# Performance work log

Hardware: AMD Instinct MI355X
Metric: run time of the kernel (lower is better)

## Reference

```python
import jax, jax.numpy as jnp
import numpy as np
from jax import lax

T, H = 4096, 2048          # tokens, hidden_size
E, K = 64, 8               # n_routed_experts, top_k
I = 512                    # moe_intermediate_size
IS = 512                   # shared intermediate = moe_intermediate_size * n_shared_experts
ROUTED_SCALING = 2.5


def setup_inputs() -> dict:
    key = jax.random.key(0)
    ks = jax.random.split(key, 6)
    return {
        "hidden_states": jax.random.normal(ks[0], (T, H), jnp.float32),
        "gate_w": jax.random.normal(ks[1], (H, E), jnp.float32) * 0.05,
        "w13": jax.random.normal(ks[2], (E, H, 2 * I), jnp.float32) * 0.02,
        "w2": jax.random.normal(ks[3], (E, I, H), jnp.float32) * 0.02,
        "shared_w13": jax.random.normal(ks[4], (H, 2 * IS), jnp.float32) * 0.02,
        "shared_w2": jax.random.normal(ks[5], (IS, H), jnp.float32) * 0.02,
    }


def reference(hidden_states, gate_w, w13, w2, shared_w13, shared_w2):
    # --- router: sigmoid scoring, grouped top-k with 1 group == plain top-k ---
    logits = hidden_states @ gate_w                        # [T, E]
    scores = jax.nn.sigmoid(logits.astype(jnp.float32))
    topk_w, topk_ids = lax.top_k(scores, K)                # [T, K]
    topk_w = topk_w / jnp.sum(topk_w, axis=-1, keepdims=True)  # renormalize

    # --- dispatch: sort token-expert pairs by expert id, grouped GEMM ---
    flat_ids = topk_ids.reshape(-1)                        # [T*K]
    order = jnp.argsort(flat_ids)                          # pairs grouped by expert
    token_idx = order // K                                 # source token of each sorted pair
    x_sorted = hidden_states[token_idx]                    # [T*K, H]
    group_sizes = jnp.bincount(flat_ids, length=E).astype(jnp.int32)

    gu = lax.ragged_dot(x_sorted, w13, group_sizes)        # [T*K, 2I]
    h = jax.nn.silu(gu[:, :I]) * gu[:, I:]                 # SiluAndMul
    out_sorted = lax.ragged_dot(h, w2, group_sizes)        # [T*K, H]

    # --- combine: unsort, weight, sum over top-k ---
    inv = jnp.argsort(order)
    out_pairs = out_sorted[inv].reshape(T, K, H)
    routed = jnp.sum(out_pairs * topk_w[..., None].astype(out_pairs.dtype), axis=1)

    # --- shared expert MLP ---
    sg = hidden_states @ shared_w13                        # [T, 2*IS]
    shared = (jax.nn.silu(sg[:, :IS]) * sg[:, IS:]) @ shared_w2

    return routed * ROUTED_SCALING + shared
```

## Files before the change

### kernel.cpp

```cpp
#include <hip/hip_runtime.h>
#include <hip/hip_bf16.h>

#define T_TOK 4096
#define HD    2048
#define NE    64
#define TOPK  8
#define IMID  512
#define N13   1024
#define NPAIR (T_TOK*TOPK)
#define NROWS (NPAIR + T_TOK)
#define MAXT2 208
#define RSCALE 2.5f

typedef __attribute__((ext_vector_type(8))) __bf16 bf16x8;
typedef __attribute__((ext_vector_type(4))) __bf16 bf16x4;
typedef __attribute__((ext_vector_type(4))) float  f32x4;

__global__ __launch_bounds__(256) void init_kernel(float4* __restrict__ out4,
                                                   int* __restrict__ counts,
                                                   int* __restrict__ curs) {
  int gid = blockIdx.x * 256 + threadIdx.x;
  float4 z; z.x = z.y = z.z = z.w = 0.f;
  out4[gid] = z;
  if (gid < NE + 1) { counts[gid] = 0; curs[gid] = 0; }
}

__global__ __launch_bounds__(256) void cvt_kernel(const float4* __restrict__ hs4,
                                                  bf16x8* __restrict__ hb8) {
  int gid = blockIdx.x * 256 + threadIdx.x;
  float4 a = hs4[2 * gid], b = hs4[2 * gid + 1];
  bf16x8 v = { (__bf16)a.x, (__bf16)a.y, (__bf16)a.z, (__bf16)a.w,
               (__bf16)b.x, (__bf16)b.y, (__bf16)b.z, (__bf16)b.w };
  hb8[gid] = v;
}

__global__ __launch_bounds__(256) void logits_kernel(const float* __restrict__ hs,
                                                     const float* __restrict__ gw,
                                                     float* __restrict__ logits) {
  __shared__ float hsm[64][64];
  __shared__ float gwm[64][64];
  int tid = threadIdx.x;
  int tb = blockIdx.x * 64;
  int tok = tid & 63, kq = tid >> 6;
  int tq = (tid & 15) * 4, eq = (tid >> 4) * 4;
  float acc[4][4] = {};
  for (int c = 0; c < 32; ++c) {
    int kb = c * 64;
#pragma unroll
    for (int it = 0; it < 4; ++it) {
      int k4 = kq * 16 + it * 4;
      float4 f = *(const float4*)&hs[(size_t)(tb + tok) * HD + kb + k4];
      hsm[k4 + 0][tok] = f.x; hsm[k4 + 1][tok] = f.y;
      hsm[k4 + 2][tok] = f.z; hsm[k4 + 3][tok] = f.w;
      int q = tid + it * 256;
      int grow = q >> 4, gc = (q & 15) * 4;
      *(float4*)&gwm[grow][gc] = *(const float4*)&gw[(size_t)(kb + grow) * NE + gc];
    }
    __syncthreads();
#pragma unroll 8
    for (int k = 0; k < 64; ++k) {
      float4 g = *(const float4*)&gwm[k][eq];
      float h0 = hsm[k][tq + 0], h1 = hsm[k][tq + 1];
      float h2 = hsm[k][tq + 2], h3 = hsm[k][tq + 3];
      acc[0][0] += h0 * g.x; acc[0][1] += h0 * g.y; acc[0][2] += h0 * g.z; acc[0][3] += h0 * g.w;
      acc[1][0] += h1 * g.x; acc[1][1] += h1 * g.y; acc[1][2] += h1 * g.z; acc[1][3] += h1 * g.w;
      acc[2][0] += h2 * g.x; acc[2][1] += h2 * g.y; acc[2][2] += h2 * g.z; acc[2][3] += h2 * g.w;
      acc[3][0] += h3 * g.x; acc[3][1] += h3 * g.y; acc[3][2] += h3 * g.z; acc[3][3] += h3 * g.w;
    }
    __syncthreads();
  }
#pragma unroll
  for (int i = 0; i < 4; ++i)
#pragma unroll
    for (int j = 0; j < 4; ++j)
      logits[(size_t)(tb + tq + i) * NE + eq + j] = acc[i][j];
}

__global__ __launch_bounds__(256) void top8_kernel(const float* __restrict__ logits,
                                                   int* __restrict__ topk_id,
                                                   float* __restrict__ pair_w,
                                                   int* __restrict__ counts) {
  int lane = threadIdx.x & 63;
  int t = blockIdx.x * 4 + (threadIdx.x >> 6);
  float v = logits[(size_t)t * NE + lane];
  float s = 1.f / (1.f + __expf(-v));
  float cur = s, ssum = 0.f;
  int myid = 0; float myw = 0.f;
  for (int k = 0; k < TOPK; ++k) {
    float bv = cur; int bi = lane;
#pragma unroll
    for (int off = 32; off >= 1; off >>= 1) {
      float ov = __shfl_xor(bv, off);
      int   oi = __shfl_xor(bi, off);
      if (ov > bv || (ov == bv && oi < bi)) { bv = ov; bi = oi; }
    }
    ssum += bv;
    if (lane == k) { myid = bi; myw = bv; }
    if (lane == bi) cur = -1.f;
  }
  if (lane < TOPK) {
    topk_id[(size_t)t * TOPK + lane] = myid;
    pair_w[(size_t)t * TOPK + lane] = myw / ssum * RSCALE;
    atomicAdd(&counts[myid], 1);
  }
}

__global__ void scan_kernel(int* __restrict__ counts, int* __restrict__ offs,
                            int2* __restrict__ tiles) {
  if (threadIdx.x != 0) return;
  counts[NE] = T_TOK;
  int off = 0, tix = 0;
  for (int e = 0; e <= NE; ++e) {
    offs[e] = off;
    int c = counts[e];
    int nt = (c + 255) >> 8;
    for (int i = 0; i < nt; ++i) {
      int rr = c - i * 256; if (rr > 256) rr = 256;
      tiles[tix++] = make_int2(off + i * 256, (e << 16) | rr);
    }
    off += c;
  }
  for (; tix < MAXT2; ++tix) tiles[tix] = make_int2(0, 0);
}

__global__ __launch_bounds__(256) void scatter_kernel(const int* __restrict__ topk_id,
                                                      const float* __restrict__ pair_w,
                                                      const int* __restrict__ offs,
                                                      int* __restrict__ curs,
                                                      int* __restrict__ row_token,
                                                      float* __restrict__ row_w) {
  int p = blockIdx.x * 256 + threadIdx.x;
  int dst, t; float w;
  if (p < NPAIR) {
    t = p >> 3; int e = topk_id[p]; w = pair_w[p];
    dst = offs[e] + atomicAdd(&curs[e], 1);
  } else {
    t = p - NPAIR; w = 1.0f;
    dst = offs[NE] + t;
  }
  row_token[dst] = t;
  row_w[dst] = w;
}

__device__ __forceinline__ int swz(int row, int kbyte) {
  return row * 128 + (kbyte ^ ((row & 7) << 4));
}
__device__ __forceinline__ void barrier_lgkm() {
  asm volatile("s_waitcnt lgkmcnt(0)" ::: "memory");
  __builtin_amdgcn_s_barrier();
  __builtin_amdgcn_sched_barrier(0);
}
__device__ __forceinline__ void barrier_plain() {
  __builtin_amdgcn_sched_barrier(0);
  __builtin_amdgcn_s_barrier();
  __builtin_amdgcn_sched_barrier(0);
}
__device__ __forceinline__ void wait_vm0() {
  asm volatile("s_waitcnt vmcnt(0)" ::: "memory");
}
__device__ __forceinline__ void glds16(const void* g, void* l) {
  __builtin_amdgcn_global_load_lds((const __attribute__((address_space(1))) void*)g,
                                   (__attribute__((address_space(3))) void*)l, 16, 0, 0);
}
__device__ __forceinline__ void store_b4(__bf16* Bs, int c2, int kbyte, const float2* p) {
  bf16x4 c0 = { (__bf16)p[0].x, (__bf16)p[1].x, (__bf16)p[2].x, (__bf16)p[3].x };
  bf16x4 c1 = { (__bf16)p[0].y, (__bf16)p[1].y, (__bf16)p[2].y, (__bf16)p[3].y };
  *(bf16x4*)&Bs[swz(c2,     kbyte) >> 1] = c0;
  *(bf16x4*)&Bs[swz(c2 + 1, kbyte) >> 1] = c1;
}
__device__ __forceinline__ void store_b8(__bf16* Bs, int c2, int kbyte, const float2* p) {
  bf16x8 c0 = { (__bf16)p[0].x, (__bf16)p[1].x, (__bf16)p[2].x, (__bf16)p[3].x,
                (__bf16)p[4].x, (__bf16)p[5].x, (__bf16)p[6].x, (__bf16)p[7].x };
  bf16x8 c1 = { (__bf16)p[0].y, (__bf16)p[1].y, (__bf16)p[2].y, (__bf16)p[3].y,
                (__bf16)p[4].y, (__bf16)p[5].y, (__bf16)p[6].y, (__bf16)p[7].y };
  *(bf16x8*)&Bs[swz(c2,     kbyte) >> 1] = c0;
  *(bf16x8*)&Bs[swz(c2 + 1, kbyte) >> 1] = c1;
}

__global__ __launch_bounds__(512, 4) void gemm1_kernel(const __bf16* __restrict__ hidden_bf,
                                                       const float* __restrict__ w13,
                                                       const float* __restrict__ sw13,
                                                       const int* __restrict__ row_token,
                                                       const int2* __restrict__ tiles,
                                                       __bf16* __restrict__ hbuf) {
  int2 td = tiles[blockIdx.y];
  int rows = td.y & 0xFFFF;
  if (rows == 0) return;
  int e = td.y >> 16, row0 = td.x;
  const float* W = (e < NE) ? (w13 + (size_t)e * (HD * N13)) : sw13;
  int n0 = blockIdx.x * 64;

  __shared__ __bf16 As[256 * 64];
  __shared__ __bf16 Bgs[2][64 * 64];
  __shared__ __bf16 Bus[2][64 * 64];

  int tid = threadIdx.x;
  int lane = tid & 63, wv = tid >> 6;
  int l15 = lane & 15, lq = lane >> 4;

  int kswz = (((lane & 7) ^ (lane >> 3)) << 3);
  const __bf16* Abase[4];
#pragma unroll
  for (int i = 0; i < 4; ++i) {
    int grow = row0 + wv * 32 + i * 8 + (lane >> 3);
    if (grow >= NROWS) grow = NROWS - 1;
    Abase[i] = hidden_bf + (size_t)row_token[grow] * HD + kswz;
  }
  int c2 = (tid & 31) * 2, kq = tid >> 5;
  const float* Bg0 = W + (size_t)(kq * 4) * N13 + n0 + c2;
  const float* Bu0 = Bg0 + 512;

  float2 pg[4], pu[4];
#pragma unroll
  for (int r = 0; r < 4; ++r) {
    pg[r] = *(const float2*)(Bg0 + (size_t)r * N13);
    pu[r] = *(const float2*)(Bu0 + (size_t)r * N13);
  }
#pragma unroll
  for (int i = 0; i < 4; ++i)
    glds16(Abase[i], &As[wv * 2048 + i * 512]);
  store_b4(Bgs[0], c2, kq * 8, pg);
  store_b4(Bus[0], c2, kq * 8, pu);
  wait_vm0();
  barrier_lgkm();

  f32x4 accg[2][4], accu[2][4];
#pragma unroll
  for (int i = 0; i < 2; ++i)
#pragma unroll
    for (int j = 0; j < 4; ++j) { accg[i][j] = (f32x4)(0.f); accu[i][j] = (f32x4)(0.f); }

  for (int s = 0; s < 32; ++s) {
    int cur = s & 1;
    if (s + 1 < 32) {
      const float* Bg2 = Bg0 + (size_t)(s + 1) * 64 * N13;
      const float* Bu2 = Bu0 + (size_t)(s + 1) * 64 * N13;
#pragma unroll
      for (int r = 0; r < 4; ++r) {
        pg[r] = *(const float2*)(Bg2 + (size_t)r * N13);
        pu[r] = *(const float2*)(Bu2 + (size_t)r * N13);
      }
    }
#pragma unroll
    for (int kk = 0; kk < 2; ++kk) {
      int koff = kk * 64 + lq * 16;
      bf16x8 a0 = *(const bf16x8*)&As[swz(wv * 32 + l15,      koff) >> 1];
      bf16x8 a1 = *(const bf16x8*)&As[swz(wv * 32 + 16 + l15, koff) >> 1];
      {
        bf16x8 b[4];
#pragma unroll
        for (int j = 0; j < 4; ++j) b[j] = *(const bf16x8*)&Bgs[cur][swz(j * 16 + l15, koff) >> 1];
#pragma unroll
        for (int j = 0; j < 4; ++j) {
          accg[0][j] = __builtin_amdgcn_mfma_f32_16x16x32_bf16(a0, b[j], accg[0][j], 0, 0, 0);
          accg[1][j] = __builtin_amdgcn_mfma_f32_16x16x32_bf16(a1, b[j], accg[1][j], 0, 0, 0);
        }
      }
      {
        bf16x8 b[4];
#pragma unroll
        for (int j = 0; j < 4; ++j) b[j] = *(const bf16x8*)&Bus[cur][swz(j * 16 + l15, koff) >> 1];
#pragma unroll
        for (int j = 0; j < 4; ++j) {
          accu[0][j] = __builtin_amdgcn_mfma_f32_16x16x32_bf16(a0, b[j], accu[0][j], 0, 0, 0);
          accu[1][j] = __builtin_amdgcn_mfma_f32_16x16x32_bf16(a1, b[j], accu[1][j], 0, 0, 0);
        }
      }
    }
    barrier_plain();
    if (s + 1 < 32) {
#pragma unroll
      for (int i = 0; i < 4; ++i)
        glds16(Abase[i] + (s + 1) * 64, &As[wv * 2048 + i * 512]);
      store_b4(Bgs[cur ^ 1], c2, kq * 8, pg);
      store_b4(Bus[cur ^ 1], c2, kq * 8, pu);
      wait_vm0();
    }
    barrier_lgkm();
  }
#pragma unroll
  for (int mi = 0; mi < 2; ++mi) {
#pragma unroll
    for (int r = 0; r < 4; ++r) {
      int rl = wv * 32 + mi * 16 + lq * 4 + r;
      if (rl < rows) {
        size_t hrow = (size_t)(row0 + rl) * IMID;
#pragma unroll
        for (int j = 0; j < 4; ++j) {
          float g = accg[mi][j][r], u = accu[mi][j][r];
          float hv = g * u / (1.f + __expf(-g));
          hbuf[hrow + n0 + j * 16 + l15] = (__bf16)hv;
        }
      }
    }
  }
}

__global__ __launch_bounds__(512, 4) void gemm2_kernel(const __bf16* __restrict__ hbuf,
                                                       const float* __restrict__ w2,
                                                       const float* __restrict__ sw2,
                                                       const int* __restrict__ row_token,
                                                       const float* __restrict__ row_w,
                                                       const int2* __restrict__ tiles,
                                                       float* __restrict__ out) {
  int2 td = tiles[blockIdx.y];
  int rows = td.y & 0xFFFF;
  if (rows == 0) return;
  int e = td.y >> 16, row0 = td.x;
  const float* W = (e < NE) ? (w2 + (size_t)e * (IMID * HD)) : sw2;
  int n0 = blockIdx.x * 128;

  __shared__ __bf16 As[256 * 64];
  __shared__ __bf16 Bs[2][128 * 64];

  int tid = threadIdx.x;
  int lane = tid & 63, wv = tid >> 6, wr = wv >> 1, wc = wv & 1;
  int l15 = lane & 15, lq = lane >> 4;

  int kswz = (((lane & 7) ^ (lane >> 3)) << 3);
  const __bf16* Abase[4];
#pragma unroll
  for (int i = 0; i < 4; ++i) {
    int grow = row0 + wv * 32 + i * 8 + (lane >> 3);
    if (grow >= NROWS) grow = NROWS - 1;
    Abase[i] = hbuf + (size_t)grow * IMID + kswz;
  }

  int c2 = (tid & 63) * 2, kq = tid >> 6;
  const float* Bp0 = W + (size_t)(kq * 8) * HD + n0 + c2;

  float2 pb[8];
#pragma unroll
  for (int r = 0; r < 8; ++r) pb[r] = *(const float2*)(Bp0 + (size_t)r * HD);
#pragma unroll
  for (int i = 0; i < 4; ++i)
    glds16(Abase[i], &As[wv * 2048 + i * 512]);
  store_b8(Bs[0], c2, kq * 16, pb);
  wait_vm0();
  barrier_lgkm();

  f32x4 acc[4][4];
#pragma unroll
  for (int i = 0; i < 4; ++i)
#pragma unroll
    for (int j = 0; j < 4; ++j) acc[i][j] = (f32x4)(0.f);

  for (int s = 0; s < 8; ++s) {
    int cur = s & 1;
    if (s + 1 < 8) {
      const float* Bp2 = Bp0 + (size_t)(s + 1) * 64 * HD;
#pragma unroll
      for (int r = 0; r < 8; ++r) pb[r] = *(const float2*)(Bp2 + (size_t)r * HD);
    }
#pragma unroll
    for (int kk = 0; kk < 2; ++kk) {
      int koff = kk * 64 + lq * 16;
      bf16x8 a[4];
#pragma unroll
      for (int i = 0; i < 4; ++i)
        a[i] = *(const bf16x8*)&As[swz(wr * 64 + i * 16 + l15, koff) >> 1];
#pragma unroll
      for (int j = 0; j < 4; ++j) {
        bf16x8 b = *(const bf16x8*)&Bs[cur][swz(wc * 64 + j * 16 + l15, koff) >> 1];
#pragma unroll
        for (int i = 0; i < 4; ++i)
          acc[i][j] = __builtin_amdgcn_mfma_f32_16x16x32_bf16(a[i], b, acc[i][j], 0, 0, 0);
      }
    }
    barrier_plain();
    if (s + 1 < 8) {
#pragma unroll
      for (int i = 0; i < 4; ++i)
        glds16(Abase[i] + (s + 1) * 64, &As[wv * 2048 + i * 512]);
      store_b8(Bs[cur ^ 1], c2, kq * 16, pb);
      wait_vm0();
    }
    barrier_lgkm();
  }
#pragma unroll
  for (int i = 0; i < 4; ++i) {
#pragma unroll
    for (int r = 0; r < 4; ++r) {
      int rl = wr * 64 + i * 16 + lq * 4 + r;
      if (rl < rows) {
        int gr = row0 + rl;
        int tok = row_token[gr];
        float wgt = row_w[gr];
        float* orow = out + (size_t)tok * HD + n0 + wc * 64;
#pragma unroll
        for (int j = 0; j < 4; ++j)
          atomicAdd(&orow[j * 16 + l15], acc[i][j][r] * wgt);
      }
    }
  }
}

extern "C" void kernel_launch(void* const* d_in, const int* in_sizes, int n_in,
                              void* d_out, int out_size, void* d_ws, size_t ws_size,
                              hipStream_t stream) {
  const float* hidden = (const float*)d_in[0];
  const float* gate_w = (const float*)d_in[1];
  const float* w13    = (const float*)d_in[2];
  const float* w2     = (const float*)d_in[3];
  const float* sw13   = (const float*)d_in[4];
  const float* sw2    = (const float*)d_in[5];
  float* out = (float*)d_out;

  char* ws = (char*)d_ws;
  size_t off = 0;
  __bf16* hbuf      = (__bf16*)(ws + off); off += (size_t)NROWS * IMID * 2;
  __bf16* hidden_bf = (__bf16*)(ws + off); off += (size_t)T_TOK * HD * 2;
  float* logits  = (float*)(ws + off);  off += (size_t)T_TOK * NE * 4;
  int*   topk_id = (int*)(ws + off);    off += (size_t)NPAIR * 4;
  float* pair_w  = (float*)(ws + off);  off += (size_t)NPAIR * 4;
  int*   row_tok = (int*)(ws + off);    off += (size_t)NROWS * 4;
  float* row_w   = (float*)(ws + off);  off += (size_t)NROWS * 4;
  int*   counts  = (int*)(ws + off);    off += 512;
  int*   curs    = (int*)(ws + off);    off += 512;
  int*   offs    = (int*)(ws + off);    off += 512;
  int2*  tiles   = (int2*)(ws + off);   off += MAXT2 * 8;

  init_kernel<<<T_TOK * HD / 4 / 256, 256, 0, stream>>>((float4*)out, counts, curs);
  cvt_kernel<<<T_TOK * HD / 8 / 256, 256, 0, stream>>>((const float4*)hidden, (bf16x8*)hidden_bf);
  logits_kernel<<<T_TOK / 64, 256, 0, stream>>>(hidden, gate_w, logits);
  top8_kernel<<<T_TOK / 4, 256, 0, stream>>>(logits, topk_id, pair_w, counts);
  scan_kernel<<<1, 64, 0, stream>>>(counts, offs, tiles);
  scatter_kernel<<<NROWS / 256, 256, 0, stream>>>(topk_id, pair_w, offs, curs, row_tok, row_w);
  gemm1_kernel<<<dim3(8, MAXT2), 512, 0, stream>>>(hidden_bf, w13, sw13, row_tok, tiles, hbuf);
  gemm2_kernel<<<dim3(16, MAXT2), 512, 0, stream>>>(hbuf, w2, sw2, row_tok, row_w, tiles, out);
}
```

Measured before the change: 829.0 us.

## Triple-buffer A tiles, single barrier per k-step, retile gemm1 warps

```diff
diff --git a/kernel.cpp b/kernel.cpp
--- a/kernel.cpp
+++ b/kernel.cpp
@@ -145,19 +145,6 @@
 __device__ __forceinline__ int swz(int row, int kbyte) {
   return row * 128 + (kbyte ^ ((row & 7) << 4));
 }
-__device__ __forceinline__ void barrier_lgkm() {
-  asm volatile("s_waitcnt lgkmcnt(0)" ::: "memory");
-  __builtin_amdgcn_s_barrier();
-  __builtin_amdgcn_sched_barrier(0);
-}
-__device__ __forceinline__ void barrier_plain() {
-  __builtin_amdgcn_sched_barrier(0);
-  __builtin_amdgcn_s_barrier();
-  __builtin_amdgcn_sched_barrier(0);
-}
-__device__ __forceinline__ void wait_vm0() {
-  asm volatile("s_waitcnt vmcnt(0)" ::: "memory");
-}
 __device__ __forceinline__ void glds16(const void* g, void* l) {
   __builtin_amdgcn_global_load_lds((const __attribute__((address_space(1))) void*)g,
                                    (__attribute__((address_space(3))) void*)l, 16, 0, 0);
@@ -177,7 +164,7 @@
   *(bf16x8*)&Bs[swz(c2 + 1, kbyte) >> 1] = c1;
 }
 
-__global__ __launch_bounds__(512, 4) void gemm1_kernel(const __bf16* __restrict__ hidden_bf,
+__global__ __launch_bounds__(512, 2) void gemm1_kernel(const __bf16* __restrict__ hidden_bf,
                                                        const float* __restrict__ w13,
                                                        const float* __restrict__ sw13,
                                                        const int* __restrict__ row_token,
@@ -190,12 +177,13 @@
   const float* W = (e < NE) ? (w13 + (size_t)e * (HD * N13)) : sw13;
   int n0 = blockIdx.x * 64;
 
-  __shared__ __bf16 As[256 * 64];
+  __shared__ __bf16 As[3][256 * 64];
   __shared__ __bf16 Bgs[2][64 * 64];
   __shared__ __bf16 Bus[2][64 * 64];
 
   int tid = threadIdx.x;
   int lane = tid & 63, wv = tid >> 6;
+  int wrow = wv >> 1, wc = wv & 1;
   int l15 = lane & 15, lq = lane >> 4;
 
   int kswz = (((lane & 7) ^ (lane >> 3)) << 3);
@@ -216,22 +204,24 @@
     pg[r] = *(const float2*)(Bg0 + (size_t)r * N13);
     pu[r] = *(const float2*)(Bu0 + (size_t)r * N13);
   }
-#pragma unroll
-  for (int i = 0; i < 4; ++i)
-    glds16(Abase[i], &As[wv * 2048 + i * 512]);
   store_b4(Bgs[0], c2, kq * 8, pg);
   store_b4(Bus[0], c2, kq * 8, pu);
-  wait_vm0();
-  barrier_lgkm();
-
-  f32x4 accg[2][4], accu[2][4];
-#pragma unroll
-  for (int i = 0; i < 2; ++i)
-#pragma unroll
-    for (int j = 0; j < 4; ++j) { accg[i][j] = (f32x4)(0.f); accu[i][j] = (f32x4)(0.f); }
+#pragma unroll
+  for (int i = 0; i < 4; ++i) glds16(Abase[i],      &As[0][wv * 2048 + i * 512]);
+#pragma unroll
+  for (int i = 0; i < 4; ++i) glds16(Abase[i] + 64, &As[1][wv * 2048 + i * 512]);
+  asm volatile("s_waitcnt vmcnt(0) lgkmcnt(0)" ::: "memory");
+  __builtin_amdgcn_s_barrier();
+  __builtin_amdgcn_sched_barrier(0);
+
+  f32x4 accg[4][2], accu[4][2];
+#pragma unroll
+  for (int i = 0; i < 4; ++i)
+#pragma unroll
+    for (int j = 0; j < 2; ++j) { accg[i][j] = (f32x4)(0.f); accu[i][j] = (f32x4)(0.f); }
 
   for (int s = 0; s < 32; ++s) {
-    int cur = s & 1;
+    int cur = s % 3, nb = s & 1;
     if (s + 1 < 32) {
       const float* Bg2 = Bg0 + (size_t)(s + 1) * 64 * N13;
       const float* Bu2 = Bu0 + (size_t)(s + 1) * 64 * N13;
@@ -241,62 +231,63 @@
         pu[r] = *(const float2*)(Bu2 + (size_t)r * N13);
       }
     }
+    if (s + 2 < 32) {
+      int nxt3 = (s + 2) % 3;
+#pragma unroll
+      for (int i = 0; i < 4; ++i)
+        glds16(Abase[i] + (s + 2) * 64, &As[nxt3][wv * 2048 + i * 512]);
+    }
+    __builtin_amdgcn_sched_barrier(0);
 #pragma unroll
     for (int kk = 0; kk < 2; ++kk) {
       int koff = kk * 64 + lq * 16;
-      bf16x8 a0 = *(const bf16x8*)&As[swz(wv * 32 + l15,      koff) >> 1];
-      bf16x8 a1 = *(const bf16x8*)&As[swz(wv * 32 + 16 + l15, koff) >> 1];
-      {
-        bf16x8 b[4];
-#pragma unroll
-        for (int j = 0; j < 4; ++j) b[j] = *(const bf16x8*)&Bgs[cur][swz(j * 16 + l15, koff) >> 1];
-#pragma unroll
-        for (int j = 0; j < 4; ++j) {
-          accg[0][j] = __builtin_amdgcn_mfma_f32_16x16x32_bf16(a0, b[j], accg[0][j], 0, 0, 0);
-          accg[1][j] = __builtin_amdgcn_mfma_f32_16x16x32_bf16(a1, b[j], accg[1][j], 0, 0, 0);
+      bf16x8 a[4], bg[2], bu[2];
+#pragma unroll
+      for (int i = 0; i < 4; ++i)
+        a[i] = *(const bf16x8*)&As[cur][swz(wrow * 64 + i * 16 + l15, koff) >> 1];
+#pragma unroll
+      for (int j = 0; j < 2; ++j) {
+        bg[j] = *(const bf16x8*)&Bgs[nb][swz(wc * 32 + j * 16 + l15, koff) >> 1];
+        bu[j] = *(const bf16x8*)&Bus[nb][swz(wc * 32 + j * 16 + l15, koff) >> 1];
+      }
+#pragma unroll
+      for (int i = 0; i < 4; ++i)
+#pragma unroll
+        for (int j = 0; j < 2; ++j) {
+          accg[i][j] = __builtin_amdgcn_mfma_f32_16x16x32_bf16(a[i], bg[j], accg[i][j], 0, 0, 0);
+          accu[i][j] = __builtin_amdgcn_mfma_f32_16x16x32_bf16(a[i], bu[j], accu[i][j], 0, 0, 0);
+        }
+    }
+    if (s + 1 < 32) {
+      store_b4(Bgs[nb ^ 1], c2, kq * 8, pg);
+      store_b4(Bus[nb ^ 1], c2, kq * 8, pu);
+    }
+    if (s + 2 < 32)
+      asm volatile("s_waitcnt vmcnt(4) lgkmcnt(0)" ::: "memory");
+    else
+      asm volatile("s_waitcnt vmcnt(0) lgkmcnt(0)" ::: "memory");
+    __builtin_amdgcn_s_barrier();
+    __builtin_amdgcn_sched_barrier(0);
+  }
+#pragma unroll
+  for (int mi = 0; mi < 4; ++mi) {
+#pragma unroll
+    for (int r = 0; r < 4; ++r) {
+      int rl = wrow * 64 + mi * 16 + lq * 4 + r;
+      if (rl < rows) {
+        size_t hrow = (size_t)(row0 + rl) * IMID;
+#pragma unroll
+        for (int j = 0; j < 2; ++j) {
+          float g = accg[mi][j][r], u = accu[mi][j][r];
+          float hv = g * u / (1.f + __expf(-g));
+          hbuf[hrow + n0 + wc * 32 + j * 16 + l15] = (__bf16)hv;
         }
       }
-      {
-        bf16x8 b[4];
-#pragma unroll
-        for (int j = 0; j < 4; ++j) b[j] = *(const bf16x8*)&Bus[cur][swz(j * 16 + l15, koff) >> 1];
-#pragma unroll
-        for (int j = 0; j < 4; ++j) {
-          accu[0][j] = __builtin_amdgcn_mfma_f32_16x16x32_bf16(a0, b[j], accu[0][j], 0, 0, 0);
-          accu[1][j] = __builtin_amdgcn_mfma_f32_16x16x32_bf16(a1, b[j], accu[1][j], 0, 0, 0);
-        }
-      }
-    }
-    barrier_plain();
-    if (s + 1 < 32) {
-#pragma unroll
-      for (int i = 0; i < 4; ++i)
-        glds16(Abase[i] + (s + 1) * 64, &As[wv * 2048 + i * 512]);
-      store_b4(Bgs[cur ^ 1], c2, kq * 8, pg);
-      store_b4(Bus[cur ^ 1], c2, kq * 8, pu);
-      wait_vm0();
-    }
-    barrier_lgkm();
-  }
-#pragma unroll
-  for (int mi = 0; mi < 2; ++mi) {
-#pragma unroll
-    for (int r = 0; r < 4; ++r) {
-      int rl = wv * 32 + mi * 16 + lq * 4 + r;
-      if (rl < rows) {
-        size_t hrow = (size_t)(row0 + rl) * IMID;
-#pragma unroll
-        for (int j = 0; j < 4; ++j) {
-          float g = accg[mi][j][r], u = accu[mi][j][r];
-          float hv = g * u / (1.f + __expf(-g));
-          hbuf[hrow + n0 + j * 16 + l15] = (__bf16)hv;
-        }
-      }
-    }
-  }
-}
-
-__global__ __launch_bounds__(512, 4) void gemm2_kernel(const __bf16* __restrict__ hbuf,
+    }
+  }
+}
+
+__global__ __launch_bounds__(512, 2) void gemm2_kernel(const __bf16* __restrict__ hbuf,
                                                        const float* __restrict__ w2,
                                                        const float* __restrict__ sw2,
                                                        const int* __restrict__ row_token,
@@ -310,7 +301,7 @@
   const float* W = (e < NE) ? (w2 + (size_t)e * (IMID * HD)) : sw2;
   int n0 = blockIdx.x * 128;
 
-  __shared__ __bf16 As[256 * 64];
+  __shared__ __bf16 As[3][256 * 64];
   __shared__ __bf16 Bs[2][128 * 64];
 
   int tid = threadIdx.x;
@@ -332,50 +323,57 @@
   float2 pb[8];
 #pragma unroll
   for (int r = 0; r < 8; ++r) pb[r] = *(const float2*)(Bp0 + (size_t)r * HD);
+  store_b8(Bs[0], c2, kq * 16, pb);
+#pragma unroll
+  for (int i = 0; i < 4; ++i) glds16(Abase[i],      &As[0][wv * 2048 + i * 512]);
+#pragma unroll
+  for (int i = 0; i < 4; ++i) glds16(Abase[i] + 64, &As[1][wv * 2048 + i * 512]);
+  asm volatile("s_waitcnt vmcnt(0) lgkmcnt(0)" ::: "memory");
+  __builtin_amdgcn_s_barrier();
+  __builtin_amdgcn_sched_barrier(0);
+
+  f32x4 acc[4][4];
 #pragma unroll
   for (int i = 0; i < 4; ++i)
-    glds16(Abase[i], &As[wv * 2048 + i * 512]);
-  store_b8(Bs[0], c2, kq * 16, pb);
-  wait_vm0();
-  barrier_lgkm();
-
-  f32x4 acc[4][4];
-#pragma unroll
-  for (int i = 0; i < 4; ++i)
 #pragma unroll
     for (int j = 0; j < 4; ++j) acc[i][j] = (f32x4)(0.f);
 
   for (int s = 0; s < 8; ++s) {
-    int cur = s & 1;
+    int cur = s % 3, nb = s & 1;
     if (s + 1 < 8) {
       const float* Bp2 = Bp0 + (size_t)(s + 1) * 64 * HD;
 #pragma unroll
       for (int r = 0; r < 8; ++r) pb[r] = *(const float2*)(Bp2 + (size_t)r * HD);
     }
+    if (s + 2 < 8) {
+      int nxt3 = (s + 2) % 3;
+#pragma unroll
+      for (int i = 0; i < 4; ++i)
+        glds16(Abase[i] + (s + 2) * 64, &As[nxt3][wv * 2048 + i * 512]);
+    }
+    __builtin_amdgcn_sched_barrier(0);
 #pragma unroll
     for (int kk = 0; kk < 2; ++kk) {
       int koff = kk * 64 + lq * 16;
       bf16x8 a[4];
 #pragma unroll
       for (int i = 0; i < 4; ++i)
-        a[i] = *(const bf16x8*)&As[swz(wr * 64 + i * 16 + l15, koff) >> 1];
+        a[i] = *(const bf16x8*)&As[cur][swz(wr * 64 + i * 16 + l15, koff) >> 1];
 #pragma unroll
       for (int j = 0; j < 4; ++j) {
-        bf16x8 b = *(const bf16x8*)&Bs[cur][swz(wc * 64 + j * 16 + l15, koff) >> 1];
+        bf16x8 b = *(const bf16x8*)&Bs[nb][swz(wc * 64 + j * 16 + l15, koff) >> 1];
 #pragma unroll
         for (int i = 0; i < 4; ++i)
           acc[i][j] = __builtin_amdgcn_mfma_f32_16x16x32_bf16(a[i], b, acc[i][j], 0, 0, 0);
       }
     }
-    barrier_plain();
-    if (s + 1 < 8) {
-#pragma unroll
-      for (int i = 0; i < 4; ++i)
-        glds16(Abase[i] + (s + 1) * 64, &As[wv * 2048 + i * 512]);
-      store_b8(Bs[cur ^ 1], c2, kq * 16, pb);
-      wait_vm0();
-    }
-    barrier_lgkm();
+    if (s + 1 < 8) store_b8(Bs[nb ^ 1], c2, kq * 16, pb);
+    if (s + 2 < 8)
+      asm volatile("s_waitcnt vmcnt(4) lgkmcnt(0)" ::: "memory");
+    else
+      asm volatile("s_waitcnt vmcnt(0) lgkmcnt(0)" ::: "memory");
+    __builtin_amdgcn_s_barrier();
+    __builtin_amdgcn_sched_barrier(0);
   }
 #pragma unroll
   for (int i = 0; i < 4; ++i) {
```

New measurement: 1.023 ms. +23.4%, slower.
